# Optimization experiments

Hardware: AMD Instinct MI355X
Metric: run time of the kernel (lower is better)

The kernel has to match this reference:

```python
import jax, jax.numpy as jnp
import numpy as np

N = 50000       # nodes
E = 800000      # edges (avg degree 16)
C_IN = 128
C_HID = 64
C_OUT = 64
NEG_SLOPE = 0.2  # PyG GATConv default


def setup_inputs() -> dict:
    key = jax.random.key(0)
    ks = jax.random.split(key, 20)
    inp = {
        "x": jax.random.normal(ks[0], (N, C_IN), dtype=jnp.float32),
        "edge_index": jax.random.randint(ks[1], (2, E), 0, N, dtype=jnp.int32),
        "batch_size": N,
        "framework": 1,
    }
    dims = [(C_IN, C_HID), (C_HID, C_HID), (C_HID, C_OUT)]
    k = 2
    for i, (cin, cout) in enumerate(dims):
        s = 1.0 / np.sqrt(cin)
        inp[f"W{i}"] = jax.random.normal(ks[k], (cin, cout), jnp.float32) * s; k += 1
        inp[f"a_src{i}"] = jax.random.normal(ks[k], (cout,), jnp.float32) * (1.0 / np.sqrt(cout)); k += 1
        inp[f"a_dst{i}"] = jax.random.normal(ks[k], (cout,), jnp.float32) * (1.0 / np.sqrt(cout)); k += 1
        inp[f"b{i}"] = jnp.zeros((cout,), jnp.float32); k += 1
    return inp


def _gat_conv(h, src, dst, n, W, a_src, a_dst, b):
    # h: [n, cin] -> [n, cout]; single head, PyG GATConv semantics
    hp = h @ W                                   # [n, cout]
    alpha_s = hp @ a_src                         # [n]
    alpha_d = hp @ a_dst                         # [n]
    e = alpha_s[src] + alpha_d[dst]              # [E'] per-edge logits
    e = jnp.where(e > 0, e, NEG_SLOPE * e)       # leaky_relu(0.2)
    # segment softmax over incoming edges of each destination node
    m = jax.ops.segment_max(e, dst, num_segments=n)
    e = jnp.exp(e - m[dst])
    denom = jax.ops.segment_sum(e, dst, num_segments=n)
    a = e / (denom[dst] + 1e-16)                 # [E']
    msg = hp[src] * a[:, None]                   # [E', cout]
    out = jax.ops.segment_sum(msg, dst, num_segments=n)
    return out + b


def reference(x, edge_index, batch_size, framework,
              W0, a_src0, a_dst0, b0,
              W1, a_src1, a_dst1, b1,
              W2, a_src2, a_dst2, b2):
    n = x.shape[0]
    loops = jnp.arange(n, dtype=edge_index.dtype)  # PyG add_self_loops=True
    src = jnp.concatenate([edge_index[0], loops])
    dst = jnp.concatenate([edge_index[1], loops])
    params = [(W0, a_src0, a_dst0, b0), (W1, a_src1, a_dst1, b1), (W2, a_src2, a_dst2, b2)]
    h = x
    for W, a_s, a_d, b in params:
        h = jax.nn.relu(_gat_conv(h, src, dst, n, W, a_s, a_d, b))
    if framework:
        return h
    return h[:batch_size]
```

## Files before the change

kernel.cpp:

```cpp
#include <hip/hip_runtime.h>
#include <hip/hip_fp16.h>
#include <math.h>

#define NEG_SLOPE 0.2f
#define BSHIFT 8
#define BCAP 8192

typedef __attribute__((ext_vector_type(8))) short bf16x8;
typedef __attribute__((ext_vector_type(4))) float f32x4;

__device__ __forceinline__ float leaky(float e) {
    return e > 0.f ? e : NEG_SLOPE * e;
}
__device__ __forceinline__ float to_f(float x) { return x; }
__device__ __forceinline__ float to_f(__half x) { return __half2float(x); }

__device__ __forceinline__ unsigned f2bf_bits(float x) {
    unsigned u = __float_as_uint(x);
    return (u + 0x7fffu + ((u >> 16) & 1u)) >> 16;
}


__global__ __launch_bounds__(256) void pack_w3_kernel(
        const float* __restrict__ W0, const float* __restrict__ W1,
        const float* __restrict__ W2, short* __restrict__ Whi,
        short* __restrict__ Wlo, int* __restrict__ bucketLen) {
    int idx = blockIdx.x * 256 + threadIdx.x;
    if (idx < 256) bucketLen[idx] = 0;
    if (idx >= 16384) return;
    const float* W;
    int base, li;
    if (idx < 8192)       { W = W0; base = 0;     li = idx; }
    else if (idx < 12288) { W = W1; base = 8192;  li = idx - 8192; }
    else                  { W = W2; base = 12288; li = idx - 12288; }
    int k = li >> 6, col = li & 63;
    int c = k >> 5, kin = k & 31;
    int g = col >> 4, nn = col & 15;
    float x = W[li];
    unsigned hb = f2bf_bits(x);
    float hf = __uint_as_float(hb << 16);
    unsigned lb = f2bf_bits(x - hf);
    int o = base + (((c * 4 + g) * 16 + nn) << 5) + kin;
    Whi[o] = (short)hb;
    Wlo[o] = (short)lb;
}


__global__ __launch_bounds__(256) void partition_kernel(
        const int* __restrict__ src, const int* __restrict__ dst,
        int* __restrict__ bucketLen, int* __restrict__ pairs, int E, int nbk) {
    __shared__ int cnt[256];
    __shared__ int run[256];
    int t = threadIdx.x;
    int chunk = (E + gridDim.x - 1) / gridDim.x;
    int beg = blockIdx.x * chunk;
    int end = min(beg + chunk, E);
    cnt[t] = 0;
    __syncthreads();
    for (int i = beg + t; i < end; i += 256)
        atomicAdd(&cnt[dst[i] >> BSHIFT], 1);
    __syncthreads();
    if (t < nbk) run[t] = t * BCAP + atomicAdd(&bucketLen[t], cnt[t]);
    __syncthreads();
    for (int i = beg + t; i < end; i += 256) {
        int d = dst[i];
        int slot = atomicAdd(&run[d >> BSHIFT], 1);
        if (slot < (d >> BSHIFT) * BCAP + BCAP)
            pairs[slot] = (src[i] << BSHIFT) | (d & 255);
    }
}

__device__ void csr_build_body(
        int b, const int* __restrict__ bucketLen, const int* __restrict__ pairs,
        int* __restrict__ off, int* __restrict__ degA,
        int* __restrict__ csr_src, int N) {
    __shared__ int degl[256];
    __shared__ int s[256];
    __shared__ int cur[256];
    int t = threadIdx.x;
    int n0 = b << BSHIFT;
    int nodecnt = min(256, N - n0);
    int ebeg = b * BCAP;
    int eend = ebeg + bucketLen[b];

    degl[t] = 0;
    __syncthreads();
    for (int i = ebeg + t; i < eend; i += 256)
        atomicAdd(&degl[pairs[i] & 255], 1);
    __syncthreads();

    int v = degl[t];
    s[t] = v;
    __syncthreads();
    for (int o = 1; o < 256; o <<= 1) {
        int x = (t >= o) ? s[t - o] : 0;
        __syncthreads();
        s[t] += x;
        __syncthreads();
    }
    int excl = s[t] - v;
    if (t < nodecnt) {
        off[n0 + t] = ebeg + excl;
        degA[n0 + t] = v;
    }
    cur[t] = excl;
    __syncthreads();

    for (int i = ebeg + t; i < eend; i += 256) {
        int pk = pairs[i];
        int p = atomicAdd(&cur[pk & 255], 1);
        csr_src[ebeg + p] = pk >> BSHIFT;
    }
}


template <int CIN, typename InT>
__device__ void gemm_body(
        int bid, const InT* __restrict__ h, const short* __restrict__ Whi,
        const short* __restrict__ Wlo,
        const float* __restrict__ a_src, const float* __restrict__ a_dst,
        __half* __restrict__ hp, float* __restrict__ as_, float* __restrict__ ad_,
        int n) {
    constexpr int KC = CIN / 32;
    int t = threadIdx.x, wave = t >> 6, lane = t & 63;
    int quad = lane >> 4, l16 = lane & 15;
    int node0 = bid * 64 + wave * 16;

    f32x4 acc[4];
#pragma unroll
    for (int g = 0; g < 4; ++g) acc[g] = (f32x4){0.f, 0.f, 0.f, 0.f};

    int nodeA = node0 + l16;
    bool va = nodeA < n;
    const InT* hrow = h + (size_t)(va ? nodeA : 0) * CIN + quad * 8;

#pragma unroll
    for (int c = 0; c < KC; ++c) {
        bf16x8 bhi[4], blo[4];
#pragma unroll
        for (int g = 0; g < 4; ++g) {
            int o = (((c * 4 + g) * 16 + l16) << 5) + quad * 8;
            bhi[g] = *(const bf16x8*)(Whi + o);
            blo[g] = *(const bf16x8*)(Wlo + o);
        }
        bf16x8 ahi, alo;
#pragma unroll
        for (int j = 0; j < 8; ++j) {
            float x = va ? to_f(hrow[c * 32 + j]) : 0.f;
            unsigned hb = f2bf_bits(x);
            float hf = __uint_as_float(hb << 16);
            unsigned lb = f2bf_bits(x - hf);
            ahi[j] = (short)hb;
            alo[j] = (short)lb;
        }
#pragma unroll
        for (int g = 0; g < 4; ++g) {
            acc[g] = __builtin_amdgcn_mfma_f32_16x16x32_bf16(ahi, bhi[g], acc[g], 0, 0, 0);
            acc[g] = __builtin_amdgcn_mfma_f32_16x16x32_bf16(ahi, blo[g], acc[g], 0, 0, 0);
            acc[g] = __builtin_amdgcn_mfma_f32_16x16x32_bf16(alo, bhi[g], acc[g], 0, 0, 0);
        }
    }

    float as4[4], ad4[4];
#pragma unroll
    for (int g = 0; g < 4; ++g) {
        as4[g] = a_src[g * 16 + l16];
        ad4[g] = a_dst[g * 16 + l16];
    }
#pragma unroll
    for (int r = 0; r < 4; ++r) {
        int node = node0 + quad * 4 + r;
        bool v = node < n;
        float vs = 0.f, vd = 0.f;
#pragma unroll
        for (int g = 0; g < 4; ++g) {
            float val = acc[g][r];
            if (v) hp[(size_t)node * 64 + g * 16 + l16] = __float2half_rn(val);
            vs = fmaf(val, as4[g], vs);
            vd = fmaf(val, ad4[g], vd);
        }
#pragma unroll
        for (int o = 1; o <= 8; o <<= 1) {
            vs += __shfl_xor(vs, o);
            vd += __shfl_xor(vd, o);
        }
        if (v && l16 == 0) {
            as_[node] = vs;
            ad_[node] = vd;
        }
    }
}


__device__ __forceinline__ void h8_to_f(uint4 u, float* f) {
    __half2 a = *(__half2*)&u.x;
    __half2 b = *(__half2*)&u.y;
    __half2 c = *(__half2*)&u.z;
    __half2 d = *(__half2*)&u.w;
    float2 f01 = __half22float2(a);
    float2 f23 = __half22float2(b);
    float2 f45 = __half22float2(c);
    float2 f67 = __half22float2(d);
    f[0] = f01.x; f[1] = f01.y; f[2] = f23.x; f[3] = f23.y;
    f[4] = f45.x; f[5] = f45.y; f[6] = f67.x; f[7] = f67.y;
}

__device__ __forceinline__ void store8(__half* out, size_t node, int s8, const float* v) {
    __half2 h0 = __floats2half2_rn(v[0], v[1]);
    __half2 h1 = __floats2half2_rn(v[2], v[3]);
    __half2 h2 = __floats2half2_rn(v[4], v[5]);
    __half2 h3 = __floats2half2_rn(v[6], v[7]);
    uint4 u;
    u.x = *(unsigned*)&h0; u.y = *(unsigned*)&h1;
    u.z = *(unsigned*)&h2; u.w = *(unsigned*)&h3;
    ((uint4*)out)[node * 8 + s8] = u;
}
__device__ __forceinline__ void store8(float* out, size_t node, int s8, const float* v) {
    float4 a, b;
    a.x = v[0]; a.y = v[1]; a.z = v[2]; a.w = v[3];
    b.x = v[4]; b.y = v[5]; b.z = v[6]; b.w = v[7];
    ((float4*)out)[node * 16 + s8 * 2] = a;
    ((float4*)out)[node * 16 + s8 * 2 + 1] = b;
}
__device__ __forceinline__ void store_el(float* out, size_t idx, float v) { out[idx] = v; }
__device__ __forceinline__ void store_el(__half* out, size_t idx, float v) { out[idx] = __float2half_rn(v); }

template <typename OutT>
__device__ void agg_body(
        int node, const __half* __restrict__ hp,
        const float* __restrict__ as_, const float* __restrict__ ad_,
        const int* __restrict__ off, const int* __restrict__ degA,
        const int* __restrict__ csr_src,
        const float* __restrict__ bias, OutT* __restrict__ out, int n) {
    __shared__ float pw[4][64];
    __shared__ int ps[4][64];
    int t = threadIdx.x;
    int wave = t >> 6, lane = t & 63;
    int hf = lane >> 5, l32 = lane & 31;
    if (node >= n) return;

    int beg = off[node];
    int deg = degA[node];
    float adst = ad_[node];
    float e_self = leaky(as_[node] + adst);

    if (deg <= 32) {
        bool valid = l32 < deg;
        int s = valid ? csr_src[beg + l32] : 0;
        ps[wave][lane] = s;

        int g8 = l32 >> 3, s8 = l32 & 7;
        int base = hf * 32;
        const uint4* hp4 = (const uint4*)hp;

        uint4 u8[8];
#pragma unroll
        for (int q = 0; q < 8; ++q) {
            int jj = g8 + 4 * q;
            if (jj < deg) {
                int sj = ps[wave][base + jj];
                u8[q] = hp4[(size_t)sj * 8 + s8];
            }
        }
        uint4 uself = (g8 == 0) ? hp4[(size_t)node * 8 + s8]
                                : make_uint4(0u, 0u, 0u, 0u);

        float e = valid ? leaky(as_[s] + adst) : -3.4e38f;
        float m = e;
#pragma unroll
        for (int o = 16; o > 0; o >>= 1) m = fmaxf(m, __shfl_xor(m, o));
        m = fmaxf(m, e_self);

        float p = valid ? __expf(e - m) : 0.f;
        float pself = __expf(e_self - m);
        float se = p;
#pragma unroll
        for (int o = 16; o > 0; o >>= 1) se += __shfl_xor(se, o);
        se += pself;
        float inv = 1.0f / (se + 1e-16f);
        pw[wave][lane] = p * inv;

        float acc[8];
        float wself = (g8 == 0) ? pself * inv : 0.f;
        {
            float fs[8];
            h8_to_f(uself, fs);
#pragma unroll
            for (int i = 0; i < 8; ++i) acc[i] = wself * fs[i];
        }
#pragma unroll
        for (int q = 0; q < 8; ++q) {
            int jj = g8 + 4 * q;
            if (jj < deg) {
                float w = pw[wave][base + jj];
                float f8[8];
                h8_to_f(u8[q], f8);
#pragma unroll
                for (int i = 0; i < 8; ++i) acc[i] = fmaf(w, f8[i], acc[i]);
            }
        }

#pragma unroll
        for (int i = 0; i < 8; ++i) {
            acc[i] += __shfl_xor(acc[i], 8);
            acc[i] += __shfl_xor(acc[i], 16);
        }

        if (g8 == 0) {
            const float4* b4 = (const float4*)bias;
            float4 ba = b4[s8 * 2], bb = b4[s8 * 2 + 1];
            float v[8];
            v[0] = acc[0] + ba.x; v[1] = acc[1] + ba.y;
            v[2] = acc[2] + ba.z; v[3] = acc[3] + ba.w;
            v[4] = acc[4] + bb.x; v[5] = acc[5] + bb.y;
            v[6] = acc[6] + bb.z; v[7] = acc[7] + bb.w;
#pragma unroll
            for (int i = 0; i < 8; ++i) v[i] = v[i] > 0.f ? v[i] : 0.f;
            store8(out, (size_t)node, s8, v);
        }
    } else {
        int end = beg + deg;
        float mymax = e_self;
        for (int i = beg + l32; i < end; i += 32) {
            int s = csr_src[i];
            mymax = fmaxf(mymax, leaky(as_[s] + adst));
        }
#pragma unroll
        for (int o = 16; o > 0; o >>= 1) mymax = fmaxf(mymax, __shfl_xor(mymax, o));
        float m = mymax;

        float se = 0.f;
        for (int i = beg + l32; i < end; i += 32) {
            int s = csr_src[i];
            se += __expf(leaky(as_[s] + adst) - m);
        }
#pragma unroll
        for (int o = 16; o > 0; o >>= 1) se += __shfl_xor(se, o);
        se += __expf(e_self - m);
        float inv = 1.0f / (se + 1e-16f);

        const __half2* hpx = (const __half2*)hp;
        float2 hs = __half22float2(hpx[(size_t)node * 32 + l32]);
        float wself = __expf(e_self - m) * inv;
        float a0 = wself * hs.x, a1 = wself * hs.y;
        for (int i = beg; i < end; ++i) {
            int s = csr_src[i];
            float w = __expf(leaky(as_[s] + adst) - m) * inv;
            float2 hv = __half22float2(hpx[(size_t)s * 32 + l32]);
            a0 = fmaf(w, hv.x, a0);
            a1 = fmaf(w, hv.y, a1);
        }
        float r0 = a0 + bias[l32 * 2];
        float r1 = a1 + bias[l32 * 2 + 1];
        store_el(out, (size_t)node * 64 + l32 * 2,     r0 > 0.f ? r0 : 0.f);
        store_el(out, (size_t)node * 64 + l32 * 2 + 1, r1 > 0.f ? r1 : 0.f);
    }
}


__global__ __launch_bounds__(256) void csr_gemm0_kernel(
        const int* __restrict__ bucketLen, const int* __restrict__ pairs,
        int* __restrict__ off, int* __restrict__ degA, int* __restrict__ csr_src,
        int N, int nbk,
        const float* __restrict__ x, const short* __restrict__ Whi,
        const short* __restrict__ Wlo, const float* __restrict__ a_src,
        const float* __restrict__ a_dst, __half* __restrict__ hp,
        float* __restrict__ as_, float* __restrict__ ad_) {
    if ((int)blockIdx.x < nbk)
        csr_build_body(blockIdx.x, bucketLen, pairs, off, degA, csr_src, N);
    else
        gemm_body<128, float>((int)blockIdx.x - nbk, x, Whi, Wlo,
                              a_src, a_dst, hp, as_, ad_, N);
}

template <int CIN, typename InT>
__global__ __launch_bounds__(256) void gemm_mfma_kernel(
        const InT* __restrict__ h, const short* __restrict__ Whi,
        const short* __restrict__ Wlo,
        const float* __restrict__ a_src, const float* __restrict__ a_dst,
        __half* __restrict__ hp, float* __restrict__ as_, float* __restrict__ ad_,
        int n) {
    gemm_body<CIN, InT>((int)blockIdx.x, h, Whi, Wlo, a_src, a_dst, hp, as_, ad_, n);
}

template <typename OutT>
__global__ __launch_bounds__(256) void agg_kernel(
        const __half* __restrict__ hp,
        const float* __restrict__ as_, const float* __restrict__ ad_,
        const int* __restrict__ off, const int* __restrict__ degA,
        const int* __restrict__ csr_src,
        const float* __restrict__ bias, OutT* __restrict__ out, int n) {
    int t = threadIdx.x;
    int wave = t >> 6, lane = t & 63;
    int hf = lane >> 5;
    int node = blockIdx.x * 8 + wave * 2 + hf;
    agg_body<OutT>(node, hp, as_, ad_, off, degA, csr_src, bias, out, n);
}


extern "C" void kernel_launch(void* const* d_in, const int* in_sizes, int n_in,
                              void* d_out, int out_size, void* d_ws, size_t ws_size,
                              hipStream_t stream) {
    const float* x = (const float*)d_in[0];
    const int* edge_index = (const int*)d_in[1];
    const int N = in_sizes[0] / 128;
    const int E = in_sizes[1] / 2;
    const int NBK = (N + 255) >> BSHIFT;

    const float* W[3]    = {(const float*)d_in[4], (const float*)d_in[8],  (const float*)d_in[12]};
    const float* asrc[3] = {(const float*)d_in[5], (const float*)d_in[9],  (const float*)d_in[13]};
    const float* adst[3] = {(const float*)d_in[6], (const float*)d_in[10], (const float*)d_in[14]};
    const float* bias[3] = {(const float*)d_in[7], (const float*)d_in[11], (const float*)d_in[15]};

    char* ws = (char*)d_ws;
    size_t o = 0;
    auto alloc = [&](size_t bytes) {
        char* p = ws + o;
        o += (bytes + 255) & ~(size_t)255;
        return p;
    };
    int* bucketLen    = (int*)alloc(256 * 4);
    int* pairs        = (int*)alloc((size_t)NBK * BCAP * 4);
    int* off          = (int*)alloc((size_t)N * 4);
    int* degA         = (int*)alloc((size_t)N * 4);
    int* csr_src      = (int*)alloc((size_t)NBK * BCAP * 4);
    float* as_        = (float*)alloc((size_t)N * 4);
    float* ad_        = (float*)alloc((size_t)N * 4);
    __half* hpbuf     = (__half*)alloc((size_t)N * 64 * 2);
    __half* actB      = (__half*)alloc((size_t)N * 64 * 2);
    short* Whi        = (short*)alloc(16384 * 2);
    short* Wlo        = (short*)alloc(16384 * 2);

    const int* srcp = edge_index;
    const int* dstp = edge_index + E;

    int gb = (N + 63) / 64;
    int ab = (N + 7) / 8;

    pack_w3_kernel<<<64, 256, 0, stream>>>(W[0], W[1], W[2], Whi, Wlo, bucketLen);
    partition_kernel<<<1024, 256, 0, stream>>>(srcp, dstp, bucketLen, pairs, E, NBK);

    csr_gemm0_kernel<<<NBK + gb, 256, 0, stream>>>(
        bucketLen, pairs, off, degA, csr_src, N, NBK,
        x, Whi, Wlo, asrc[0], adst[0], hpbuf, as_, ad_);
    agg_kernel<__half><<<ab, 256, 0, stream>>>(
        hpbuf, as_, ad_, off, degA, csr_src, bias[0], actB, N);

    gemm_mfma_kernel<64, __half><<<gb, 256, 0, stream>>>(
        actB, Whi + 8192, Wlo + 8192, asrc[1], adst[1], hpbuf, as_, ad_, N);
    agg_kernel<__half><<<ab, 256, 0, stream>>>(
        hpbuf, as_, ad_, off, degA, csr_src, bias[1], actB, N);

    gemm_mfma_kernel<64, __half><<<gb, 256, 0, stream>>>(
        actB, Whi + 12288, Wlo + 12288, asrc[2], adst[2], hpbuf, as_, ad_, N);
    agg_kernel<float><<<ab, 256, 0, stream>>>(
        hpbuf, as_, ad_, off, degA, csr_src, bias[2], (float*)d_out, N);
}
```

Baseline: 265.9 us.

## Fuse next-layer GEMM and attention logits into aggregation kernel, merge pack with partition

Each aggregation kernel now multiplies its output row by the next layer's weight matrix, which is staged in shared memory as fp32. In the same pass it writes the next hp, alpha_src and alpha_dst, so the separate MFMA GEMM launches and the activation round trip through global memory are gone. The weight packing is cut down to W0 only and merged with the edge partition into one launch, and a memset clears bucketLen. The costs are 16KB of shared memory per block, scalar FMAs replacing the MFMA path for layers 1 and 2, and ping-pong buffers so reads and writes do not alias.

```diff
diff --git a/kernel.cpp b/kernel.cpp
--- a/kernel.cpp
+++ b/kernel.cpp
@@ -21,18 +21,9 @@
 }
 
 
-__global__ __launch_bounds__(256) void pack_w3_kernel(
-        const float* __restrict__ W0, const float* __restrict__ W1,
-        const float* __restrict__ W2, short* __restrict__ Whi,
-        short* __restrict__ Wlo, int* __restrict__ bucketLen) {
-    int idx = blockIdx.x * 256 + threadIdx.x;
-    if (idx < 256) bucketLen[idx] = 0;
-    if (idx >= 16384) return;
-    const float* W;
-    int base, li;
-    if (idx < 8192)       { W = W0; base = 0;     li = idx; }
-    else if (idx < 12288) { W = W1; base = 8192;  li = idx - 8192; }
-    else                  { W = W2; base = 12288; li = idx - 12288; }
+__device__ __forceinline__ void pack_body_w0(
+        int li, const float* __restrict__ W, short* __restrict__ Whi,
+        short* __restrict__ Wlo) {
     int k = li >> 6, col = li & 63;
     int c = k >> 5, kin = k & 31;
     int g = col >> 4, nn = col & 15;
@@ -40,20 +31,21 @@
     unsigned hb = f2bf_bits(x);
     float hf = __uint_as_float(hb << 16);
     unsigned lb = f2bf_bits(x - hf);
-    int o = base + (((c * 4 + g) * 16 + nn) << 5) + kin;
+    int o = (((c * 4 + g) * 16 + nn) << 5) + kin;
     Whi[o] = (short)hb;
     Wlo[o] = (short)lb;
 }
 
 
-__global__ __launch_bounds__(256) void partition_kernel(
+__device__ void partition_body(
         const int* __restrict__ src, const int* __restrict__ dst,
-        int* __restrict__ bucketLen, int* __restrict__ pairs, int E, int nbk) {
+        int* __restrict__ bucketLen, int* __restrict__ pairs, int E, int nbk,
+        int pb, int nb) {
     __shared__ int cnt[256];
     __shared__ int run[256];
     int t = threadIdx.x;
-    int chunk = (E + gridDim.x - 1) / gridDim.x;
-    int beg = blockIdx.x * chunk;
+    int chunk = (E + nb - 1) / nb;
+    int beg = pb * chunk;
     int end = min(beg + chunk, E);
     cnt[t] = 0;
     __syncthreads();
@@ -67,6 +59,20 @@
         int slot = atomicAdd(&run[d >> BSHIFT], 1);
         if (slot < (d >> BSHIFT) * BCAP + BCAP)
             pairs[slot] = (src[i] << BSHIFT) | (d & 255);
+    }
+}
+
+__global__ __launch_bounds__(256) void packpart_kernel(
+        const float* __restrict__ W0, short* __restrict__ Whi,
+        short* __restrict__ Wlo,
+        const int* __restrict__ src, const int* __restrict__ dst,
+        int* __restrict__ bucketLen, int* __restrict__ pairs, int E, int nbk) {
+    if ((int)blockIdx.x < 32) {
+        int idx = blockIdx.x * 256 + threadIdx.x;
+        pack_body_w0(idx, W0, Whi, Wlo);
+    } else {
+        partition_body(src, dst, bucketLen, pairs, E, nbk,
+                       (int)blockIdx.x - 32, (int)gridDim.x - 32);
     }
 }
 
@@ -190,173 +196,6 @@
         }
     }
 }
-
-
-__device__ __forceinline__ void h8_to_f(uint4 u, float* f) {
-    __half2 a = *(__half2*)&u.x;
-    __half2 b = *(__half2*)&u.y;
-    __half2 c = *(__half2*)&u.z;
-    __half2 d = *(__half2*)&u.w;
-    float2 f01 = __half22float2(a);
-    float2 f23 = __half22float2(b);
-    float2 f45 = __half22float2(c);
-    float2 f67 = __half22float2(d);
-    f[0] = f01.x; f[1] = f01.y; f[2] = f23.x; f[3] = f23.y;
-    f[4] = f45.x; f[5] = f45.y; f[6] = f67.x; f[7] = f67.y;
-}
-
-__device__ __forceinline__ void store8(__half* out, size_t node, int s8, const float* v) {
-    __half2 h0 = __floats2half2_rn(v[0], v[1]);
-    __half2 h1 = __floats2half2_rn(v[2], v[3]);
-    __half2 h2 = __floats2half2_rn(v[4], v[5]);
-    __half2 h3 = __floats2half2_rn(v[6], v[7]);
-    uint4 u;
-    u.x = *(unsigned*)&h0; u.y = *(unsigned*)&h1;
-    u.z = *(unsigned*)&h2; u.w = *(unsigned*)&h3;
-    ((uint4*)out)[node * 8 + s8] = u;
-}
-__device__ __forceinline__ void store8(float* out, size_t node, int s8, const float* v) {
-    float4 a, b;
-    a.x = v[0]; a.y = v[1]; a.z = v[2]; a.w = v[3];
-    b.x = v[4]; b.y = v[5]; b.z = v[6]; b.w = v[7];
-    ((float4*)out)[node * 16 + s8 * 2] = a;
-    ((float4*)out)[node * 16 + s8 * 2 + 1] = b;
-}
-__device__ __forceinline__ void store_el(float* out, size_t idx, float v) { out[idx] = v; }
-__device__ __forceinline__ void store_el(__half* out, size_t idx, float v) { out[idx] = __float2half_rn(v); }
-
-template <typename OutT>
-__device__ void agg_body(
-        int node, const __half* __restrict__ hp,
-        const float* __restrict__ as_, const float* __restrict__ ad_,
-        const int* __restrict__ off, const int* __restrict__ degA,
-        const int* __restrict__ csr_src,
-        const float* __restrict__ bias, OutT* __restrict__ out, int n) {
-    __shared__ float pw[4][64];
-    __shared__ int ps[4][64];
-    int t = threadIdx.x;
-    int wave = t >> 6, lane = t & 63;
-    int hf = lane >> 5, l32 = lane & 31;
-    if (node >= n) return;
-
-    int beg = off[node];
-    int deg = degA[node];
-    float adst = ad_[node];
-    float e_self = leaky(as_[node] + adst);
-
-    if (deg <= 32) {
-        bool valid = l32 < deg;
-        int s = valid ? csr_src[beg + l32] : 0;
-        ps[wave][lane] = s;
-
-        int g8 = l32 >> 3, s8 = l32 & 7;
-        int base = hf * 32;
-        const uint4* hp4 = (const uint4*)hp;
-
-        uint4 u8[8];
-#pragma unroll
-        for (int q = 0; q < 8; ++q) {
-            int jj = g8 + 4 * q;
-            if (jj < deg) {
-                int sj = ps[wave][base + jj];
-                u8[q] = hp4[(size_t)sj * 8 + s8];
-            }
-        }
-        uint4 uself = (g8 == 0) ? hp4[(size_t)node * 8 + s8]
-                                : make_uint4(0u, 0u, 0u, 0u);
-
-        float e = valid ? leaky(as_[s] + adst) : -3.4e38f;
-        float m = e;
-#pragma unroll
-        for (int o = 16; o > 0; o >>= 1) m = fmaxf(m, __shfl_xor(m, o));
-        m = fmaxf(m, e_self);
-
-        float p = valid ? __expf(e - m) : 0.f;
-        float pself = __expf(e_self - m);
-        float se = p;
-#pragma unroll
-        for (int o = 16; o > 0; o >>= 1) se += __shfl_xor(se, o);
-        se += pself;
-        float inv = 1.0f / (se + 1e-16f);
-        pw[wave][lane] = p * inv;
-
-        float acc[8];
-        float wself = (g8 == 0) ? pself * inv : 0.f;
-        {
-            float fs[8];
-            h8_to_f(uself, fs);
-#pragma unroll
-            for (int i = 0; i < 8; ++i) acc[i] = wself * fs[i];
-        }
-#pragma unroll
-        for (int q = 0; q < 8; ++q) {
-            int jj = g8 + 4 * q;
-            if (jj < deg) {
-                float w = pw[wave][base + jj];
-                float f8[8];
-                h8_to_f(u8[q], f8);
-#pragma unroll
-                for (int i = 0; i < 8; ++i) acc[i] = fmaf(w, f8[i], acc[i]);
-            }
-        }
-
-#pragma unroll
-        for (int i = 0; i < 8; ++i) {
-            acc[i] += __shfl_xor(acc[i], 8);
-            acc[i] += __shfl_xor(acc[i], 16);
-        }
-
-        if (g8 == 0) {
-            const float4* b4 = (const float4*)bias;
-            float4 ba = b4[s8 * 2], bb = b4[s8 * 2 + 1];
-            float v[8];
-            v[0] = acc[0] + ba.x; v[1] = acc[1] + ba.y;
-            v[2] = acc[2] + ba.z; v[3] = acc[3] + ba.w;
-            v[4] = acc[4] + bb.x; v[5] = acc[5] + bb.y;
-            v[6] = acc[6] + bb.z; v[7] = acc[7] + bb.w;
-#pragma unroll
-            for (int i = 0; i < 8; ++i) v[i] = v[i] > 0.f ? v[i] : 0.f;
-            store8(out, (size_t)node, s8, v);
-        }
-    } else {
-        int end = beg + deg;
-        float mymax = e_self;
-        for (int i = beg + l32; i < end; i += 32) {
-            int s = csr_src[i];
-            mymax = fmaxf(mymax, leaky(as_[s] + adst));
-        }
-#pragma unroll
-        for (int o = 16; o > 0; o >>= 1) mymax = fmaxf(mymax, __shfl_xor(mymax, o));
-        float m = mymax;
-
-        float se = 0.f;
-        for (int i = beg + l32; i < end; i += 32) {
-            int s = csr_src[i];
-            se += __expf(leaky(as_[s] + adst) - m);
-        }
-#pragma unroll
-        for (int o = 16; o > 0; o >>= 1) se += __shfl_xor(se, o);
-        se += __expf(e_self - m);
-        float inv = 1.0f / (se + 1e-16f);
-
-        const __half2* hpx = (const __half2*)hp;
-        float2 hs = __half22float2(hpx[(size_t)node * 32 + l32]);
-        float wself = __expf(e_self - m) * inv;
-        float a0 = wself * hs.x, a1 = wself * hs.y;
-        for (int i = beg; i < end; ++i) {
-            int s = csr_src[i];
-            float w = __expf(leaky(as_[s] + adst) - m) * inv;
-            float2 hv = __half22float2(hpx[(size_t)s * 32 + l32]);
-            a0 = fmaf(w, hv.x, a0);
-            a1 = fmaf(w, hv.y, a1);
-        }
-        float r0 = a0 + bias[l32 * 2];
-        float r1 = a1 + bias[l32 * 2 + 1];
-        store_el(out, (size_t)node * 64 + l32 * 2,     r0 > 0.f ? r0 : 0.f);
-        store_el(out, (size_t)node * 64 + l32 * 2 + 1, r1 > 0.f ? r1 : 0.f);
-    }
-}
-
 
 __global__ __launch_bounds__(256) void csr_gemm0_kernel(
         const int* __restrict__ bucketLen, const int* __restrict__ pairs,
@@ -373,28 +212,223 @@
                               a_src, a_dst, hp, as_, ad_, N);
 }
 
-template <int CIN, typename InT>
-__global__ __launch_bounds__(256) void gemm_mfma_kernel(
-        const InT* __restrict__ h, const short* __restrict__ Whi,
-        const short* __restrict__ Wlo,
-        const float* __restrict__ a_src, const float* __restrict__ a_dst,
-        __half* __restrict__ hp, float* __restrict__ as_, float* __restrict__ ad_,
-        int n) {
-    gemm_body<CIN, InT>((int)blockIdx.x, h, Whi, Wlo, a_src, a_dst, hp, as_, ad_, n);
-}
-
-template <typename OutT>
-__global__ __launch_bounds__(256) void agg_kernel(
-        const __half* __restrict__ hp,
-        const float* __restrict__ as_, const float* __restrict__ ad_,
+
+__device__ __forceinline__ void h8_to_f(uint4 u, float* f) {
+    __half2 a = *(__half2*)&u.x;
+    __half2 b = *(__half2*)&u.y;
+    __half2 c = *(__half2*)&u.z;
+    __half2 d = *(__half2*)&u.w;
+    float2 f01 = __half22float2(a);
+    float2 f23 = __half22float2(b);
+    float2 f45 = __half22float2(c);
+    float2 f67 = __half22float2(d);
+    f[0] = f01.x; f[1] = f01.y; f[2] = f23.x; f[3] = f23.y;
+    f[4] = f45.x; f[5] = f45.y; f[6] = f67.x; f[7] = f67.y;
+}
+
+__device__ __forceinline__ uint4 pack8h(const float* v) {
+    __half2 h0 = __floats2half2_rn(v[0], v[1]);
+    __half2 h1 = __floats2half2_rn(v[2], v[3]);
+    __half2 h2 = __floats2half2_rn(v[4], v[5]);
+    __half2 h3 = __floats2half2_rn(v[6], v[7]);
+    uint4 u;
+    u.x = *(unsigned*)&h0; u.y = *(unsigned*)&h1;
+    u.z = *(unsigned*)&h2; u.w = *(unsigned*)&h3;
+    return u;
+}
+
+template <bool FINAL>
+__global__ __launch_bounds__(256) void agg_fused_kernel(
+        const __half* __restrict__ hp_in,
+        const float* __restrict__ as_in, const float* __restrict__ ad_in,
         const int* __restrict__ off, const int* __restrict__ degA,
-        const int* __restrict__ csr_src,
-        const float* __restrict__ bias, OutT* __restrict__ out, int n) {
+        const int* __restrict__ csr_src, const float* __restrict__ bias,
+        const float* __restrict__ Wn,
+        const float* __restrict__ asn, const float* __restrict__ adn,
+        __half* __restrict__ hp_out, float* __restrict__ as_out,
+        float* __restrict__ ad_out, float* __restrict__ final_out, int n) {
+    __shared__ float pw[4][64];
+    __shared__ int ps[4][64];
+    __shared__ __half rowT[8][64];
+    __shared__ float Wl[FINAL ? 4 : 4096];
+
     int t = threadIdx.x;
+    if constexpr (!FINAL) {
+        const float4* wg = (const float4*)Wn;
+        float4* wl = (float4*)Wl;
+#pragma unroll
+        for (int i = 0; i < 4; ++i) wl[t + 256 * i] = wg[t + 256 * i];
+        __syncthreads();
+    }
+
     int wave = t >> 6, lane = t & 63;
-    int hf = lane >> 5;
+    int hf = lane >> 5, l32 = lane & 31;
     int node = blockIdx.x * 8 + wave * 2 + hf;
-    agg_body<OutT>(node, hp, as_, ad_, off, degA, csr_src, bias, out, n);
+    int slot = wave * 2 + hf;
+    if (node >= n) return;
+
+    int beg = off[node];
+    int deg = degA[node];
+    float adst = ad_in[node];
+    float e_self = leaky(as_in[node] + adst);
+
+    if (deg <= 32) {
+        bool valid = l32 < deg;
+        int s = valid ? csr_src[beg + l32] : 0;
+        ps[wave][lane] = s;
+
+        int g8 = l32 >> 3, s8 = l32 & 7;
+        int base = hf * 32;
+        const uint4* hp4 = (const uint4*)hp_in;
+
+        uint4 u8[8];
+#pragma unroll
+        for (int q = 0; q < 8; ++q) {
+            int jj = g8 + 4 * q;
+            if (jj < deg) {
+                int sj = ps[wave][base + jj];
+                u8[q] = hp4[(size_t)sj * 8 + s8];
+            }
+        }
+        uint4 uself = (g8 == 0) ? hp4[(size_t)node * 8 + s8]
+                                : make_uint4(0u, 0u, 0u, 0u);
+
+        float e = valid ? leaky(as_in[s] + adst) : -3.4e38f;
+        float m = e;
+#pragma unroll
+        for (int o = 16; o > 0; o >>= 1) m = fmaxf(m, __shfl_xor(m, o));
+        m = fmaxf(m, e_self);
+
+        float p = valid ? __expf(e - m) : 0.f;
+        float pself = __expf(e_self - m);
+        float se = p;
+#pragma unroll
+        for (int o = 16; o > 0; o >>= 1) se += __shfl_xor(se, o);
+        se += pself;
+        float inv = 1.0f / (se + 1e-16f);
+        pw[wave][lane] = p * inv;
+
+        float acc[8];
+        float wself = (g8 == 0) ? pself * inv : 0.f;
+        {
+            float fs[8];
+            h8_to_f(uself, fs);
+#pragma unroll
+            for (int i = 0; i < 8; ++i) acc[i] = wself * fs[i];
+        }
+#pragma unroll
+        for (int q = 0; q < 8; ++q) {
+            int jj = g8 + 4 * q;
+            if (jj < deg) {
+                float w = pw[wave][base + jj];
+                float f8[8];
+                h8_to_f(u8[q], f8);
+#pragma unroll
+                for (int i = 0; i < 8; ++i) acc[i] = fmaf(w, f8[i], acc[i]);
+            }
+        }
+
+#pragma unroll
+        for (int i = 0; i < 8; ++i) {
+            acc[i] += __shfl_xor(acc[i], 8);
+            acc[i] += __shfl_xor(acc[i], 16);
+        }
+
+        if (g8 == 0) {
+            const float4* b4 = (const float4*)bias;
+            float4 ba = b4[s8 * 2], bb = b4[s8 * 2 + 1];
+            float v[8];
+            v[0] = acc[0] + ba.x; v[1] = acc[1] + ba.y;
+            v[2] = acc[2] + ba.z; v[3] = acc[3] + ba.w;
+            v[4] = acc[4] + bb.x; v[5] = acc[5] + bb.y;
+            v[6] = acc[6] + bb.z; v[7] = acc[7] + bb.w;
+#pragma unroll
+            for (int i = 0; i < 8; ++i) v[i] = v[i] > 0.f ? v[i] : 0.f;
+            if constexpr (FINAL) {
+                float4 ra, rb;
+                ra.x = v[0]; ra.y = v[1]; ra.z = v[2]; ra.w = v[3];
+                rb.x = v[4]; rb.y = v[5]; rb.z = v[6]; rb.w = v[7];
+                ((float4*)final_out)[(size_t)node * 16 + s8 * 2] = ra;
+                ((float4*)final_out)[(size_t)node * 16 + s8 * 2 + 1] = rb;
+            } else {
+                ((uint4*)&rowT[slot][0])[s8] = pack8h(v);
+            }
+        }
+    } else {
+        int end = beg + deg;
+        float mymax = e_self;
+        for (int i = beg + l32; i < end; i += 32) {
+            int s = csr_src[i];
+            mymax = fmaxf(mymax, leaky(as_in[s] + adst));
+        }
+#pragma unroll
+        for (int o = 16; o > 0; o >>= 1) mymax = fmaxf(mymax, __shfl_xor(mymax, o));
+        float m = mymax;
+
+        float se = 0.f;
+        for (int i = beg + l32; i < end; i += 32) {
+            int s = csr_src[i];
+            se += __expf(leaky(as_in[s] + adst) - m);
+        }
+#pragma unroll
+        for (int o = 16; o > 0; o >>= 1) se += __shfl_xor(se, o);
+        se += __expf(e_self - m);
+        float inv = 1.0f / (se + 1e-16f);
+
+        const __half2* hpx = (const __half2*)hp_in;
+        float2 hs = __half22float2(hpx[(size_t)node * 32 + l32]);
+        float wself = __expf(e_self - m) * inv;
+        float a0 = wself * hs.x, a1 = wself * hs.y;
+        for (int i = beg; i < end; ++i) {
+            int s = csr_src[i];
+            float w = __expf(leaky(as_in[s] + adst) - m) * inv;
+            float2 hv = __half22float2(hpx[(size_t)s * 32 + l32]);
+            a0 = fmaf(w, hv.x, a0);
+            a1 = fmaf(w, hv.y, a1);
+        }
+        float r0 = a0 + bias[l32 * 2];
+        float r1 = a1 + bias[l32 * 2 + 1];
+        r0 = r0 > 0.f ? r0 : 0.f;
+        r1 = r1 > 0.f ? r1 : 0.f;
+        if constexpr (FINAL) {
+            final_out[(size_t)node * 64 + l32 * 2]     = r0;
+            final_out[(size_t)node * 64 + l32 * 2 + 1] = r1;
+        } else {
+            *(__half2*)&rowT[slot][l32 * 2] = __floats2half2_rn(r0, r1);
+        }
+    }
+
+    if constexpr (!FINAL) {
+        int c0 = l32 * 2;
+        float s0 = asn[c0], s1 = asn[c0 + 1];
+        float d0 = adn[c0], d1 = adn[c0 + 1];
+        const float2* W2p = (const float2*)Wl;
+        const uint4* row4 = (const uint4*)&rowT[slot][0];
+        float a0 = 0.f, a1 = 0.f;
+#pragma unroll
+        for (int kk = 0; kk < 8; ++kk) {
+            float f8[8];
+            h8_to_f(row4[kk], f8);
+#pragma unroll
+            for (int j = 0; j < 8; ++j) {
+                float2 w = W2p[(kk * 8 + j) * 32 + l32];
+                a0 = fmaf(f8[j], w.x, a0);
+                a1 = fmaf(f8[j], w.y, a1);
+            }
+        }
+        ((__half2*)hp_out)[(size_t)node * 32 + l32] = __floats2half2_rn(a0, a1);
+        float vs = fmaf(a0, s0, a1 * s1);
+        float vd = fmaf(a0, d0, a1 * d1);
+#pragma unroll
+        for (int o = 1; o <= 16; o <<= 1) {
+            vs += __shfl_xor(vs, o);
+            vd += __shfl_xor(vd, o);
+        }
+        if (l32 == 0) {
+            as_out[node] = vs;
+            ad_out[node] = vd;
+        }
+    }
 }
 
 
@@ -424,12 +458,14 @@
     int* off          = (int*)alloc((size_t)N * 4);
     int* degA         = (int*)alloc((size_t)N * 4);
     int* csr_src      = (int*)alloc((size_t)NBK * BCAP * 4);
-    float* as_        = (float*)alloc((size_t)N * 4);
-    float* ad_        = (float*)alloc((size_t)N * 4);
-    __half* hpbuf     = (__half*)alloc((size_t)N * 64 * 2);
-    __half* actB      = (__half*)alloc((size_t)N * 64 * 2);
-    short* Whi        = (short*)alloc(16384 * 2);
-    short* Wlo        = (short*)alloc(16384 * 2);
+    float* asA        = (float*)alloc((size_t)N * 4);
+    float* adA        = (float*)alloc((size_t)N * 4);
+    float* asB        = (float*)alloc((size_t)N * 4);
+    float* adB        = (float*)alloc((size_t)N * 4);
+    __half* hpA       = (__half*)alloc((size_t)N * 64 * 2);
+    __half* hpB       = (__half*)alloc((size_t)N * 64 * 2);
+    short* Whi        = (short*)alloc(8192 * 2);
+    short* Wlo        = (short*)alloc(8192 * 2);
 
     const int* srcp = edge_index;
     const int* dstp = edge_index + E;
@@ -437,22 +473,25 @@
     int gb = (N + 63) / 64;
     int ab = (N + 7) / 8;
 
-    pack_w3_kernel<<<64, 256, 0, stream>>>(W[0], W[1], W[2], Whi, Wlo, bucketLen);
-    partition_kernel<<<1024, 256, 0, stream>>>(srcp, dstp, bucketLen, pairs, E, NBK);
+    hipMemsetAsync(bucketLen, 0, 256 * sizeof(int), stream);
+
+    packpart_kernel<<<32 + 1024, 256, 0, stream>>>(
+        W[0], Whi, Wlo, srcp, dstp, bucketLen, pairs, E, NBK);
 
     csr_gemm0_kernel<<<NBK + gb, 256, 0, stream>>>(
         bucketLen, pairs, off, degA, csr_src, N, NBK,
-        x, Whi, Wlo, asrc[0], adst[0], hpbuf, as_, ad_);
-    agg_kernel<__half><<<ab, 256, 0, stream>>>(
-        hpbuf, as_, ad_, off, degA, csr_src, bias[0], actB, N);
-
-    gemm_mfma_kernel<64, __half><<<gb, 256, 0, stream>>>(
-        actB, Whi + 8192, Wlo + 8192, asrc[1], adst[1], hpbuf, as_, ad_, N);
-    agg_kernel<__half><<<ab, 256, 0, stream>>>(
-        hpbuf, as_, ad_, off, degA, csr_src, bias[1], actB, N);
-
-    gemm_mfma_kernel<64, __half><<<gb, 256, 0, stream>>>(
-        actB, Whi + 12288, Wlo + 12288, asrc[2], adst[2], hpbuf, as_, ad_, N);
-    agg_kernel<float><<<ab, 256, 0, stream>>>(
-        hpbuf, as_, ad_, off, degA, csr_src, bias[2], (float*)d_out, N);
-}
+        x, Whi, Wlo, asrc[0], adst[0], hpA, asA, adA);
+
+    agg_fused_kernel<false><<<ab, 256, 0, stream>>>(
+        hpA, asA, adA, off, degA, csr_src, bias[0],
+        W[1], asrc[1], adst[1], hpB, asB, adB, nullptr, N);
+
+    agg_fused_kernel<false><<<ab, 256, 0, stream>>>(
+        hpB, asB, adB, off, degA, csr_src, bias[1],
+        W[2], asrc[2], adst[2], hpA, asA, adA, nullptr, N);
+
+    agg_fused_kernel<true><<<ab, 256, 0, stream>>>(
+        hpA, asA, adA, off, degA, csr_src, bias[2],
+        nullptr, nullptr, nullptr, nullptr, nullptr, nullptr,
+        (float*)d_out, N);
+}
```

Measured after the change: 250.2 us. 5.9% less time.
